# Optimization experiments

Hardware: AMD Instinct MI355X
Metric: run time of the kernel (lower is better)

The kernel has to match this reference:

```python
import jax, jax.numpy as jnp
import numpy as np

S, B, D = 2048, 2, 2048
H, C = 16, 128  # heads, dim_head
EPS = 1e-6


def _rmsnorm(x, w):
    # per-head RMSNorm, computed in float32 like the torch module
    xf = x.astype(jnp.float32)
    var = jnp.mean(xf * xf, axis=-1, keepdims=True)
    return (xf * jax.lax.rsqrt(var + EPS) * w).astype(x.dtype)


def _rope(x, freqs):
    # x: [S,B,H,C], freqs: [S,C] raw frequencies
    cos = jnp.cos(freqs)[:, None, None, :].astype(x.dtype)
    sin = jnp.sin(freqs)[:, None, None, :].astype(x.dtype)
    x1, x2 = jnp.split(x, 2, axis=-1)
    rot = jnp.concatenate((-x2, x1), axis=-1)
    return x * cos + rot * sin


def setup_inputs() -> dict:
    key = jax.random.key(0)
    ks = jax.random.split(key, 6)
    scale = 0.02
    return {
        "x": jax.random.normal(ks[0], (S, B, D), jnp.float32),
        "rope_emb": jax.random.normal(ks[1], (S, 1, 1, C), jnp.float32),
        "Wq": jax.random.normal(ks[2], (D, D), jnp.float32) * scale,
        "Wk": jax.random.normal(ks[3], (D, D), jnp.float32) * scale,
        "Wv": jax.random.normal(ks[4], (D, D), jnp.float32) * scale,
        "Wout": jax.random.normal(ks[5], (D, D), jnp.float32) * scale,
        "q_scale": jnp.ones((C,), jnp.float32),
        "k_scale": jnp.ones((C,), jnp.float32),
    }


def reference(x, rope_emb, Wq, Wk, Wv, Wout, q_scale, k_scale):
    s, b, _ = x.shape
    freqs = rope_emb.reshape(s, C)  # squeeze(1).squeeze(1)

    # QKV projections (no bias), split heads: [S,B,H,C]
    q = (x @ Wq.T).reshape(s, b, H, C)
    k = (x @ Wk.T).reshape(s, b, H, C)
    v = (x @ Wv.T).reshape(s, b, H, C)

    # per-head RMSNorm on q, k; identity on v (qkv_norm='RRI')
    q = _rmsnorm(q, q_scale)
    k = _rmsnorm(k, k_scale)

    # RoPE on q, k (self-attention)
    q = _rope(q, freqs)
    k = _rope(k, freqs)

    # SDPA, non-causal
    inv_scale = 1.0 / jnp.sqrt(jnp.asarray(C, x.dtype))
    scores = jnp.einsum('sbnc,tbnc->bnst', q, k) * inv_scale  # [B,H,S,S]
    probs = jax.nn.softmax(scores, axis=-1)
    out = jnp.einsum('bnst,tbnc->sbnc', probs, v)  # [S,B,H,C]

    # output projection (no bias, dropout inactive)
    return out.reshape(s, b, H * C) @ Wout.T
```

## Files before the change

kernel.cpp:

```cpp
#include <hip/hip_runtime.h>
#include <stdint.h>

#define S_DIM 2048
#define B_DIM 2
#define D_DIM 2048
#define H_DIM 16
#define C_DIM 128
#define M_DIM 4096

typedef __bf16 bf16x8 __attribute__((ext_vector_type(8)));
typedef float f32x4 __attribute__((ext_vector_type(4)));
typedef unsigned short u16x8 __attribute__((ext_vector_type(8)));

__device__ __forceinline__ float bf2f(unsigned short u) {
    union { unsigned int i; float f; } c; c.i = ((unsigned int)u) << 16; return c.f;
}
__device__ __forceinline__ unsigned short f2bf(float f) {
    union { float f; unsigned int i; } c; c.f = f;
    unsigned int r = c.i + 0x7FFFu + ((c.i >> 16) & 1u);
    return (unsigned short)(r >> 16);
}

__global__ void rope_tables_k(const float* __restrict__ freqs,
                              float* __restrict__ ctab, float* __restrict__ stab, int n) {
    int i = blockIdx.x * blockDim.x + threadIdx.x;
    if (i < n) { float f = freqs[i]; ctab[i] = cosf(f); stab[i] = sinf(f); }
}

__global__ void cast_all_k(const float* __restrict__ x,
                           const float* __restrict__ w0, const float* __restrict__ w1,
                           const float* __restrict__ w2, const float* __restrict__ w3,
                           unsigned short* __restrict__ xb, unsigned short* __restrict__ wb) {
    const int nx4 = (M_DIM * D_DIM) / 4;
    const int nw4 = (D_DIM * D_DIM) / 4;
    const int total = nx4 + 4 * nw4;
    int stride = gridDim.x * blockDim.x;
    for (int i = blockIdx.x * blockDim.x + threadIdx.x; i < total; i += stride) {
        const float* src; unsigned short* dst; int idx;
        if (i < nx4) { src = x; dst = xb; idx = i; }
        else {
            int j = i - nx4;
            int sel = j >> 20;
            idx = j & (nw4 - 1);
            src = (sel == 0) ? w0 : (sel == 1) ? w1 : (sel == 2) ? w2 : w3;
            dst = wb + (size_t)sel * (size_t)D_DIM * D_DIM;
        }
        float4 v = reinterpret_cast<const float4*>(src)[idx];
        ushort4 o;
        o.x = f2bf(v.x); o.y = f2bf(v.y); o.z = f2bf(v.z); o.w = f2bf(v.w);
        reinterpret_cast<ushort4*>(dst)[idx] = o;
    }
}

template <typename OutT>
__global__ __launch_bounds__(512, 2) void gemm8_k(
    const unsigned short* __restrict__ A,
    const unsigned short* __restrict__ Bm,
    OutT* __restrict__ C,
    int M, int N, int K)
{
    constexpr int TILE = 256 * 64;
    __shared__ __align__(16) unsigned short ldsA[2][TILE];
    __shared__ __align__(16) unsigned short ldsB[2][TILE];

    const int tid  = threadIdx.x;
    const int wave = tid >> 6;
    const int lane = tid & 63;
    const int wm = wave >> 2;
    const int wn = wave & 3;
    const int g  = lane >> 4;
    const int ro = lane & 15;

    const int nwg = gridDim.x * gridDim.y;
    int lin = blockIdx.y * gridDim.x + blockIdx.x;
    lin = (lin & 7) * (nwg >> 3) + (lin >> 3);
    const int brow = (lin % gridDim.x) * 256;
    const int bcol = (lin / gridDim.x) * 256;
    const int NT = K >> 6;

    const unsigned short* As = A  + (size_t)brow * K;
    const unsigned short* Bs = Bm + (size_t)bcol * K;

    f32x4 acc[8][4] = {};

    auto stageA = [&](int T) {
        const int buf = T & 1;
        #pragma unroll
        for (int j = 0; j < 4; ++j) {
            const int slot = j * 512 + tid;
            const int row = slot >> 3, c = slot & 7;
            __builtin_amdgcn_global_load_lds(
                (const __attribute__((address_space(1))) void*)(
                    As + (size_t)row * K + T * 64 + ((c ^ (row & 7)) << 3)),
                (__attribute__((address_space(3))) void*)(
                    &ldsA[buf][(j * 512 + wave * 64) * 8]),
                16, 0, 0);
        }
    };
    auto stageB = [&](int T) {
        const int buf = T & 1;
        #pragma unroll
        for (int j = 0; j < 4; ++j) {
            const int slot = j * 512 + tid;
            const int row = slot >> 3, c = slot & 7;
            __builtin_amdgcn_global_load_lds(
                (const __attribute__((address_space(1))) void*)(
                    Bs + (size_t)row * K + T * 64 + ((c ^ (row & 7)) << 3)),
                (__attribute__((address_space(3))) void*)(
                    &ldsB[buf][(j * 512 + wave * 64) * 8]),
                16, 0, 0);
        }
    };

    auto rdA = [&](int buf, int mi, int ks) -> bf16x8 {
        const int row = wm * 128 + mi * 16 + ro;
        return *reinterpret_cast<const bf16x8*>(
            &ldsA[buf][row * 64 + (((ks * 4 + g) ^ (row & 7)) << 3)]);
    };
    auto rdB = [&](int buf, int ni, int ks) -> bf16x8 {
        const int row = wn * 64 + ni * 16 + ro;
        return *reinterpret_cast<const bf16x8*>(
            &ldsB[buf][row * 64 + (((ks * 4 + g) ^ (row & 7)) << 3)]);
    };

    stageB(0);
    stageA(0);
    stageB(1);
    asm volatile("s_waitcnt vmcnt(4)" ::: "memory");
    __builtin_amdgcn_s_barrier();

    for (int T = 0; T < NT; ++T) {
        const int buf = T & 1;
        bf16x8 af[4], bfr[4];

        #pragma unroll
        for (int i = 0; i < 4; ++i) af[i] = rdA(buf, i, 0);
        #pragma unroll
        for (int i = 0; i < 4; ++i) bfr[i] = rdB(buf, i, 0);
        if (T + 1 < NT) stageA(T + 1);
        __builtin_amdgcn_s_barrier();
        asm volatile("s_waitcnt lgkmcnt(0)" ::: "memory");
        __builtin_amdgcn_sched_barrier(0);
        __builtin_amdgcn_s_setprio(1);
        #pragma unroll
        for (int mi = 0; mi < 4; ++mi)
            #pragma unroll
            for (int ni = 0; ni < 4; ++ni)
                acc[mi][ni] = __builtin_amdgcn_mfma_f32_16x16x32_bf16(af[mi], bfr[ni], acc[mi][ni], 0, 0, 0);
        __builtin_amdgcn_s_setprio(0);
        __builtin_amdgcn_s_barrier();

        #pragma unroll
        for (int i = 0; i < 4; ++i) af[i] = rdA(buf, 4 + i, 0);
        __builtin_amdgcn_s_barrier();
        asm volatile("s_waitcnt lgkmcnt(0)" ::: "memory");
        __builtin_amdgcn_sched_barrier(0);
        __builtin_amdgcn_s_setprio(1);
        #pragma unroll
        for (int mi = 0; mi < 4; ++mi)
            #pragma unroll
            for (int ni = 0; ni < 4; ++ni)
                acc[4 + mi][ni] = __builtin_amdgcn_mfma_f32_16x16x32_bf16(af[mi], bfr[ni], acc[4 + mi][ni], 0, 0, 0);
        __builtin_amdgcn_s_setprio(0);
        __builtin_amdgcn_s_barrier();

        #pragma unroll
        for (int i = 0; i < 4; ++i) af[i] = rdA(buf, i, 1);
        #pragma unroll
        for (int i = 0; i < 4; ++i) bfr[i] = rdB(buf, i, 1);
        __builtin_amdgcn_s_barrier();
        asm volatile("s_waitcnt lgkmcnt(0)" ::: "memory");
        __builtin_amdgcn_sched_barrier(0);
        __builtin_amdgcn_s_setprio(1);
        #pragma unroll
        for (int mi = 0; mi < 4; ++mi)
            #pragma unroll
            for (int ni = 0; ni < 4; ++ni)
                acc[mi][ni] = __builtin_amdgcn_mfma_f32_16x16x32_bf16(af[mi], bfr[ni], acc[mi][ni], 0, 0, 0);
        __builtin_amdgcn_s_setprio(0);
        __builtin_amdgcn_s_barrier();

        #pragma unroll
        for (int i = 0; i < 4; ++i) af[i] = rdA(buf, 4 + i, 1);
        if (T + 2 < NT) stageB(T + 2);
        if (T + 1 < NT) {
            if (T + 2 < NT) asm volatile("s_waitcnt vmcnt(4)" ::: "memory");
            else            asm volatile("s_waitcnt vmcnt(0)" ::: "memory");
        }
        __builtin_amdgcn_s_barrier();
        asm volatile("s_waitcnt lgkmcnt(0)" ::: "memory");
        __builtin_amdgcn_sched_barrier(0);
        __builtin_amdgcn_s_setprio(1);
        #pragma unroll
        for (int mi = 0; mi < 4; ++mi)
            #pragma unroll
            for (int ni = 0; ni < 4; ++ni)
                acc[4 + mi][ni] = __builtin_amdgcn_mfma_f32_16x16x32_bf16(af[mi], bfr[ni], acc[4 + mi][ni], 0, 0, 0);
        __builtin_amdgcn_s_setprio(0);
        __builtin_amdgcn_s_barrier();
    }

    const int rg = g * 4;
    #pragma unroll
    for (int mi = 0; mi < 8; ++mi) {
        #pragma unroll
        for (int r = 0; r < 4; ++r) {
            const int row = brow + wm * 128 + mi * 16 + rg + r;
            const size_t base = (size_t)row * N + bcol + wn * 64;
            #pragma unroll
            for (int ni = 0; ni < 4; ++ni) {
                float v = acc[mi][ni][r];
                if constexpr (sizeof(OutT) == 2) C[base + ni * 16 + ro] = f2bf(v);
                else                             C[base + ni * 16 + ro] = v;
            }
        }
    }
}

template <typename OutT>
__global__ __launch_bounds__(512) void gemm_v4_k(
    const unsigned short* __restrict__ A,
    const unsigned short* __restrict__ Bm,
    OutT* __restrict__ C,
    int M, int N, int K)
{
    constexpr int ATILE = 128 * 64;
    constexpr int BTILE = 256 * 64;
    __shared__ __align__(16) unsigned short ldsA[3 * ATILE];
    __shared__ __align__(16) unsigned short ldsB[3 * BTILE];

    const int tid  = threadIdx.x;
    const int wave = tid >> 6;
    const int lane = tid & 63;
    const int wm = wave >> 2;
    const int wn = wave & 3;
    const int g  = lane >> 4;
    const int ro = lane & 15;

    const int nwg = gridDim.x * gridDim.y;
    int lin = blockIdx.y * gridDim.x + blockIdx.x;
    lin = (lin & 7) * (nwg >> 3) + (lin >> 3);
    const int brow = (lin % gridDim.x) * 128;
    const int bcol = (lin / gridDim.x) * 256;
    const int NT = K >> 6;

    const unsigned short* As = A  + (size_t)brow * K;
    const unsigned short* Bs = Bm + (size_t)bcol * K;

    f32x4 acc[4][4] = {};

    auto stage = [&](int buf, int t) {
        #pragma unroll
        for (int j = 0; j < 2; ++j) {
            const int slot = j * 512 + tid;
            const int row = slot >> 3, c = slot & 7;
            __builtin_amdgcn_global_load_lds(
                (const __attribute__((address_space(1))) void*)(
                    As + (size_t)row * K + t * 64 + ((c ^ (row & 7)) << 3)),
                (__attribute__((address_space(3))) void*)(
                    ldsA + buf * ATILE + (j * 512 + wave * 64) * 8),
                16, 0, 0);
        }
        #pragma unroll
        for (int j = 0; j < 4; ++j) {
            const int slot = j * 512 + tid;
            const int row = slot >> 3, c = slot & 7;
            __builtin_amdgcn_global_load_lds(
                (const __attribute__((address_space(1))) void*)(
                    Bs + (size_t)row * K + t * 64 + ((c ^ (row & 7)) << 3)),
                (__attribute__((address_space(3))) void*)(
                    ldsB + buf * BTILE + (j * 512 + wave * 64) * 8),
                16, 0, 0);
        }
    };

    auto rdA = [&](int buf, int mi, int ks) -> bf16x8 {
        const int row = wm * 64 + mi * 16 + ro;
        const int c = (ks * 4 + g) ^ (row & 7);
        return *reinterpret_cast<const bf16x8*>(ldsA + buf * ATILE + row * 64 + c * 8);
    };
    auto rdB = [&](int buf, int ni, int ks) -> bf16x8 {
        const int row = wn * 64 + ni * 16 + ro;
        const int c = (ks * 4 + g) ^ (row & 7);
        return *reinterpret_cast<const bf16x8*>(ldsB + buf * BTILE + row * 64 + c * 8);
    };

    stage(0, 0);
    stage(1, 1);
    asm volatile("s_waitcnt vmcnt(6)" ::: "memory");
    __builtin_amdgcn_s_barrier();

    int cb = 0;
    for (int t = 0; t < NT; ++t) {
        #pragma unroll
        for (int ks = 0; ks < 2; ++ks) {
            bf16x8 af[4], bf[4];
            #pragma unroll
            for (int i = 0; i < 4; ++i) af[i] = rdA(cb, i, ks);
            #pragma unroll
            for (int i = 0; i < 4; ++i) bf[i] = rdB(cb, i, ks);
            if (ks == 0) {
                if (t + 2 < NT) stage((cb == 0) ? 2 : cb - 1, t + 2);
            } else {
                if (t + 2 < NT) asm volatile("s_waitcnt vmcnt(6)" ::: "memory");
                else            asm volatile("s_waitcnt vmcnt(0)" ::: "memory");
            }
            __builtin_amdgcn_s_barrier();
            asm volatile("s_waitcnt lgkmcnt(0)" ::: "memory");
            __builtin_amdgcn_sched_barrier(0);
            __builtin_amdgcn_s_setprio(1);
            #pragma unroll
            for (int mi = 0; mi < 4; ++mi)
                #pragma unroll
                for (int ni = 0; ni < 4; ++ni)
                    acc[mi][ni] = __builtin_amdgcn_mfma_f32_16x16x32_bf16(
                        af[mi], bf[ni], acc[mi][ni], 0, 0, 0);
            __builtin_amdgcn_s_setprio(0);
            __builtin_amdgcn_s_barrier();
        }
        cb = (cb == 2) ? 0 : cb + 1;
    }

    const int rg = g * 4;
    #pragma unroll
    for (int mi = 0; mi < 4; ++mi) {
        #pragma unroll
        for (int r = 0; r < 4; ++r) {
            const int row = brow + wm * 64 + mi * 16 + rg + r;
            const size_t base = (size_t)row * N + bcol + wn * 64;
            #pragma unroll
            for (int ni = 0; ni < 4; ++ni) {
                float v = acc[mi][ni][r];
                if constexpr (sizeof(OutT) == 2) C[base + ni * 16 + ro] = f2bf(v);
                else                             C[base + ni * 16 + ro] = v;
            }
        }
    }
}

__global__ __launch_bounds__(256) void qk_post2_k(
    const unsigned short* __restrict__ rawQKV, int ld,
    const float* __restrict__ q_scale, const float* __restrict__ k_scale,
    const float* __restrict__ ctab, const float* __restrict__ stab,
    unsigned short* __restrict__ Qb, unsigned short* __restrict__ Kb,
    float inv_scale)
{
    const int isK = blockIdx.y;
    const unsigned short* raw = rawQKV + (isK ? D_DIM : 0);
    const float* wscale = isK ? k_scale : q_scale;
    unsigned short* outp = isK ? Kb : Qb;
    const float post_mul = isK ? 1.0f : inv_scale;

    const int gw = blockIdx.x * 4 + (threadIdx.x >> 6);
    const int lane = threadIdx.x & 63;
    const int m = gw >> 4;
    const int h = gw & 15;
    const int s = m >> 1, b = m & 1;
    const int c0 = lane * 2;

    const unsigned short* src = raw + (size_t)m * ld + h * C_DIM + c0;
    unsigned int packed = *reinterpret_cast<const unsigned int*>(src);
    float x0 = bf2f((unsigned short)(packed & 0xFFFF));
    float x1 = bf2f((unsigned short)(packed >> 16));

    float ss = x0 * x0 + x1 * x1;
    #pragma unroll
    for (int off = 32; off; off >>= 1) ss += __shfl_xor(ss, off);
    const float rs = rsqrtf(ss * (1.0f / C_DIM) + 1e-6f);

    float n0 = x0 * rs * wscale[c0];
    float n1 = x1 * rs * wscale[c0 + 1];
    float p0 = __shfl_xor(n0, 32);
    float p1 = __shfl_xor(n1, 32);
    const float sgn = (lane < 32) ? -1.0f : 1.0f;
    const float* cp = ctab + (size_t)s * C_DIM + c0;
    const float* sp = stab + (size_t)s * C_DIM + c0;
    float o0 = (n0 * cp[0] + sgn * p0 * sp[0]) * post_mul;
    float o1 = (n1 * cp[1] + sgn * p1 * sp[1]) * post_mul;

    unsigned int opk = (unsigned int)f2bf(o0) | ((unsigned int)f2bf(o1) << 16);
    *reinterpret_cast<unsigned int*>(
        outp + ((size_t)(b * H_DIM + h) * S_DIM + s) * C_DIM + c0) = opk;
}

__global__ __launch_bounds__(256) void v_transpose_k(
    const unsigned short* __restrict__ raw, int ld, int colbase,
    unsigned short* __restrict__ Vt)
{
    __shared__ __align__(16) unsigned short tile[64][136];
    const int bh = blockIdx.y;
    const int b = bh >> 4, h = bh & 15;
    const int sbase = blockIdx.x * 64;
    const int t = threadIdx.x;

    {
        const int s = t >> 2, cq = (t & 3) * 32;
        const unsigned short* src = raw + (size_t)((sbase + s) * B_DIM + b) * ld + colbase + h * C_DIM + cq;
        #pragma unroll
        for (int j = 0; j < 4; ++j) {
            u16x8 v = *reinterpret_cast<const u16x8*>(src + j * 8);
            *reinterpret_cast<u16x8*>(&tile[s][cq + j * 8]) = v;
        }
    }
    __syncthreads();
    {
        const int c = t >> 1, sh = (t & 1) * 32;
        unsigned short* dst = Vt + ((size_t)bh * C_DIM + c) * S_DIM + sbase + sh;
        #pragma unroll
        for (int j = 0; j < 32; j += 8) {
            u16x8 o;
            #pragma unroll
            for (int e = 0; e < 8; ++e) o[e] = tile[sh + j + e][c];
            *reinterpret_cast<u16x8*>(dst + j) = o;
        }
    }
}

__global__ __launch_bounds__(512, 2) void attn_k(
    const unsigned short* __restrict__ Qb,
    const unsigned short* __restrict__ Kb,
    const unsigned short* __restrict__ Vt,
    unsigned short* __restrict__ Ao)
{
    __shared__ __align__(16) unsigned short ldsK[2][64 * 128];
    __shared__ __align__(16) unsigned short ldsV[2][128 * 64];
    __shared__ __align__(16) unsigned short plds[8][32 * 64];

    const int bh = blockIdx.y;
    const int wave = threadIdx.x >> 6;
    const int lane = threadIdx.x & 63;
    const int qbase = blockIdx.x * 256 + wave * 32;
    const int g  = lane >> 4;
    const int ro = lane & 15;
    const int ko = g * 8;
    const int rg = g * 4;

    const unsigned short* Q  = Qb + (size_t)bh * S_DIM * C_DIM;
    const unsigned short* Km = Kb + (size_t)bh * S_DIM * C_DIM;
    const unsigned short* V  = Vt + (size_t)bh * C_DIM * S_DIM;
    unsigned short* pw = &plds[wave][0];

    bf16x8 qf[2][4];
    #pragma unroll
    for (int mq = 0; mq < 2; ++mq)
        #pragma unroll
        for (int kf = 0; kf < 4; ++kf)
            qf[mq][kf] = *reinterpret_cast<const bf16x8*>(
                Q + (size_t)(qbase + mq * 16 + ro) * C_DIM + kf * 32 + ko);

    bf16x8 ones;
    #pragma unroll
    for (int e = 0; e < 8; ++e) ones[e] = (__bf16)1.0f;

    auto stage = [&](int bufi, int kb) {
        #pragma unroll
        for (int j = 0; j < 2; ++j) {
            const int idx = (wave * 2 + j) * 64 + lane;
            {
                const int row = idx >> 4, ch = idx & 15;
                const int sch = (ch & 8) | ((ch ^ row) & 7);
                __builtin_amdgcn_global_load_lds(
                    (const __attribute__((address_space(1))) void*)(
                        Km + (size_t)(kb + row) * C_DIM + sch * 8),
                    (__attribute__((address_space(3))) void*)(
                        &ldsK[bufi][(wave * 2 + j) * 512]),
                    16, 0, 0);
            }
            {
                const int row = idx >> 3, ch = idx & 7;
                const int sch = (ch ^ row) & 7;
                __builtin_amdgcn_global_load_lds(
                    (const __attribute__((address_space(1))) void*)(
                        V + (size_t)row * S_DIM + kb + sch * 8),
                    (__attribute__((address_space(3))) void*)(
                        &ldsV[bufi][(wave * 2 + j) * 512]),
                    16, 0, 0);
            }
        }
    };

    f32x4 of[2][8] = {};
    f32x4 osum[2] = {};
    float mrow[2][4] = {{-1e30f, -1e30f, -1e30f, -1e30f}, {-1e30f, -1e30f, -1e30f, -1e30f}};

    stage(0, 0);
    asm volatile("s_waitcnt vmcnt(0)" ::: "memory");
    __syncthreads();

    int cur = 0;
    for (int kb = 0; kb < S_DIM; kb += 64) {
        if (kb + 64 < S_DIM) stage(cur ^ 1, kb + 64);

        f32x4 s4[2][4] = {};
        __builtin_amdgcn_s_setprio(1);
        #pragma unroll
        for (int nc = 0; nc < 4; ++nc) {
            const int r_loc = nc * 16 + ro;
            bf16x8 kfr[4];
            #pragma unroll
            for (int kf = 0; kf < 4; ++kf) {
                const int c = kf * 4 + g;
                const int sch = (c & 8) | ((c ^ r_loc) & 7);
                kfr[kf] = *reinterpret_cast<const bf16x8*>(&ldsK[cur][r_loc * 128 + sch * 8]);
            }
            #pragma unroll
            for (int mq = 0; mq < 2; ++mq)
                #pragma unroll
                for (int kf = 0; kf < 4; ++kf)
                    s4[mq][nc] = __builtin_amdgcn_mfma_f32_16x16x32_bf16(
                        qf[mq][kf], kfr[kf], s4[mq][nc], 0, 0, 0);
        }
        __builtin_amdgcn_s_setprio(0);

        float mx[2][4];
        #pragma unroll
        for (int mq = 0; mq < 2; ++mq) {
            #pragma unroll
            for (int r = 0; r < 4; ++r)
                mx[mq][r] = fmaxf(fmaxf(s4[mq][0][r], s4[mq][1][r]),
                                  fmaxf(s4[mq][2][r], s4[mq][3][r]));
            #pragma unroll
            for (int off = 1; off < 16; off <<= 1)
                #pragma unroll
                for (int r = 0; r < 4; ++r) mx[mq][r] = fmaxf(mx[mq][r], __shfl_xor(mx[mq][r], off));
        }

        float mg = 0.f;
        #pragma unroll
        for (int mq = 0; mq < 2; ++mq)
            #pragma unroll
            for (int r = 0; r < 4; ++r) mg = fmaxf(mg, mx[mq][r] - mrow[mq][r]);
        if (__any(mg > 8.0f)) {
            #pragma unroll
            for (int mq = 0; mq < 2; ++mq) {
                float resc[4];
                #pragma unroll
                for (int r = 0; r < 4; ++r) {
                    float mnew = fmaxf(mrow[mq][r], mx[mq][r]);
                    resc[r] = __expf(mrow[mq][r] - mnew);
                    mrow[mq][r] = mnew;
                    osum[mq][r] *= resc[r];
                }
                #pragma unroll
                for (int nf = 0; nf < 8; ++nf)
                    #pragma unroll
                    for (int r = 0; r < 4; ++r) of[mq][nf][r] *= resc[r];
            }
        }

        #pragma unroll
        for (int mq = 0; mq < 2; ++mq)
            #pragma unroll
            for (int nc = 0; nc < 4; ++nc)
                #pragma unroll
                for (int r = 0; r < 4; ++r) {
                    float p = __expf(s4[mq][nc][r] - mrow[mq][r]);
                    const int q = mq * 16 + rg + r;
                    const int k = nc * 16 + ro;
                    pw[q * 64 + (((k >> 3) ^ (q & 7)) << 3) + (k & 7)] = f2bf(p);
                }
        __asm__ volatile("" ::: "memory");

        __builtin_amdgcn_s_setprio(1);
        #pragma unroll
        for (int ks = 0; ks < 2; ++ks) {
            bf16x8 pa[2];
            #pragma unroll
            for (int mq = 0; mq < 2; ++mq) {
                const int prow = mq * 16 + ro;
                const int psch = (ks * 4 + g) ^ (ro & 7);
                pa[mq] = *reinterpret_cast<const bf16x8*>(&pw[prow * 64 + psch * 8]);
            }
            #pragma unroll
            for (int nf = 0; nf < 8; ++nf) {
                const int vr = nf * 16 + ro;
                const int sch = (ks * 4 + g) ^ (vr & 7);
                bf16x8 vf = *reinterpret_cast<const bf16x8*>(&ldsV[cur][vr * 64 + sch * 8]);
                #pragma unroll
                for (int mq = 0; mq < 2; ++mq)
                    of[mq][nf] = __builtin_amdgcn_mfma_f32_16x16x32_bf16(pa[mq], vf, of[mq][nf], 0, 0, 0);
            }
            #pragma unroll
            for (int mq = 0; mq < 2; ++mq)
                osum[mq] = __builtin_amdgcn_mfma_f32_16x16x32_bf16(pa[mq], ones, osum[mq], 0, 0, 0);
        }
        __builtin_amdgcn_s_setprio(0);

        asm volatile("s_waitcnt vmcnt(0)" ::: "memory");
        __syncthreads();
        cur ^= 1;
    }

    const int b = bh >> 4, h = bh & 15;
    #pragma unroll
    for (int mq = 0; mq < 2; ++mq) {
        #pragma unroll
        for (int r = 0; r < 4; ++r) {
            const float inv_l = 1.0f / osum[mq][r];
            const int srow = qbase + mq * 16 + rg + r;
            unsigned short* dst = Ao + (size_t)(srow * B_DIM + b) * D_DIM + h * C_DIM;
            #pragma unroll
            for (int nf = 0; nf < 8; ++nf)
                dst[nf * 16 + ro] = f2bf(of[mq][nf][r] * inv_l);
        }
    }
}

extern "C" void kernel_launch(void* const* d_in, const int* in_sizes, int n_in,
                              void* d_out, int out_size, void* d_ws, size_t ws_size,
                              hipStream_t stream) {
    const float* x       = (const float*)d_in[0];
    const float* rope    = (const float*)d_in[1];
    const float* Wq      = (const float*)d_in[2];
    const float* Wk      = (const float*)d_in[3];
    const float* Wv      = (const float*)d_in[4];
    const float* Wo      = (const float*)d_in[5];
    const float* q_scale = (const float*)d_in[6];
    const float* k_scale = (const float*)d_in[7];
    float* out = (float*)d_out;

    char* w = (char*)d_ws;
    size_t off = 0;
    auto alloc = [&](size_t bytes) {
        char* p = w + off; off += (bytes + 255) & ~(size_t)255; return p;
    };
    unsigned short* xb   = (unsigned short*)alloc((size_t)M_DIM * D_DIM * 2);
    unsigned short* Wqb  = (unsigned short*)alloc((size_t)4 * D_DIM * D_DIM * 2);
    unsigned short* Wob  = Wqb + (size_t)3 * D_DIM * D_DIM;
    unsigned short* rawQKV = (unsigned short*)alloc((size_t)M_DIM * 3 * D_DIM * 2);
    unsigned short* Qb   = (unsigned short*)alloc((size_t)M_DIM * D_DIM * 2);
    unsigned short* Kb   = (unsigned short*)alloc((size_t)M_DIM * D_DIM * 2);
    unsigned short* Vt   = (unsigned short*)alloc((size_t)M_DIM * D_DIM * 2);
    float* ctab = (float*)alloc((size_t)S_DIM * C_DIM * 4);
    float* stab = (float*)alloc((size_t)S_DIM * C_DIM * 4);
    unsigned short* Ao = rawQKV;
    (void)ws_size; (void)in_sizes; (void)n_in; (void)out_size;

    const int NQKV = 3 * D_DIM;
    const float inv_scale = 0.08838834764831845f;

    rope_tables_k<<<(S_DIM * C_DIM + 255) / 256, 256, 0, stream>>>(rope, ctab, stab, S_DIM * C_DIM);
    cast_all_k<<<2048, 256, 0, stream>>>(x, Wq, Wk, Wv, Wo, xb, Wqb);

    gemm8_k<unsigned short><<<dim3(M_DIM / 256, NQKV / 256), 512, 0, stream>>>(
        xb, Wqb, rawQKV, M_DIM, NQKV, D_DIM);

    qk_post2_k<<<dim3(M_DIM * H_DIM / 4, 2), 256, 0, stream>>>(
        rawQKV, NQKV, q_scale, k_scale, ctab, stab, Qb, Kb, inv_scale);
    v_transpose_k<<<dim3(S_DIM / 64, B_DIM * H_DIM), 256, 0, stream>>>(rawQKV, NQKV, 2 * D_DIM, Vt);

    attn_k<<<dim3(S_DIM / 256, B_DIM * H_DIM), 512, 0, stream>>>(Qb, Kb, Vt, Ao);

    gemm_v4_k<float><<<dim3(M_DIM / 128, D_DIM / 256), 512, 0, stream>>>(
        Ao, Wob, out, M_DIM, D_DIM, D_DIM);
}
```

Measured before the change: 343.0 us.

## Widen QKV GEMM tile to 256x384 and interleave LDS reads with MFMA

```diff
diff --git a/kernel.cpp b/kernel.cpp
--- a/kernel.cpp
+++ b/kernel.cpp
@@ -52,16 +52,18 @@
     }
 }
 
-template <typename OutT>
-__global__ __launch_bounds__(512, 2) void gemm8_k(
+template <typename OutT, int BN>
+__global__ __launch_bounds__(512) void gemm8_k(
     const unsigned short* __restrict__ A,
     const unsigned short* __restrict__ Bm,
     OutT* __restrict__ C,
     int M, int N, int K)
 {
-    constexpr int TILE = 256 * 64;
-    __shared__ __align__(16) unsigned short ldsA[2][TILE];
-    __shared__ __align__(16) unsigned short ldsB[2][TILE];
+    constexpr int NFR = BN / 64;
+    constexpr int WNS = BN / 4;
+    constexpr int BCH = BN / 64 * 512;
+    __shared__ __align__(16) unsigned short ldsA[2][256 * 64];
+    __shared__ __align__(16) unsigned short ldsB[2][BN * 64];
 
     const int tid  = threadIdx.x;
     const int wave = tid >> 6;
@@ -75,13 +77,13 @@
     int lin = blockIdx.y * gridDim.x + blockIdx.x;
     lin = (lin & 7) * (nwg >> 3) + (lin >> 3);
     const int brow = (lin % gridDim.x) * 256;
-    const int bcol = (lin / gridDim.x) * 256;
+    const int bcol = (lin / gridDim.x) * BN;
     const int NT = K >> 6;
 
     const unsigned short* As = A  + (size_t)brow * K;
     const unsigned short* Bs = Bm + (size_t)bcol * K;
 
-    f32x4 acc[8][4] = {};
+    f32x4 acc[8][NFR] = {};
 
     auto stageA = [&](int T) {
         const int buf = T & 1;
@@ -100,7 +102,7 @@
     auto stageB = [&](int T) {
         const int buf = T & 1;
         #pragma unroll
-        for (int j = 0; j < 4; ++j) {
+        for (int j = 0; j < BCH / 512; ++j) {
             const int slot = j * 512 + tid;
             const int row = slot >> 3, c = slot & 7;
             __builtin_amdgcn_global_load_lds(
@@ -118,7 +120,7 @@
             &ldsA[buf][row * 64 + (((ks * 4 + g) ^ (row & 7)) << 3)]);
     };
     auto rdB = [&](int buf, int ni, int ks) -> bf16x8 {
-        const int row = wn * 64 + ni * 16 + ro;
+        const int row = wn * WNS + ni * 16 + ro;
         return *reinterpret_cast<const bf16x8*>(
             &ldsB[buf][row * 64 + (((ks * 4 + g) ^ (row & 7)) << 3)]);
     };
@@ -126,76 +128,66 @@
     stageB(0);
     stageA(0);
     stageB(1);
-    asm volatile("s_waitcnt vmcnt(4)" ::: "memory");
+    asm volatile("s_waitcnt vmcnt(6)" ::: "memory");
     __builtin_amdgcn_s_barrier();
 
     for (int T = 0; T < NT; ++T) {
         const int buf = T & 1;
-        bf16x8 af[4], bfr[4];
-
-        #pragma unroll
-        for (int i = 0; i < 4; ++i) af[i] = rdA(buf, i, 0);
-        #pragma unroll
-        for (int i = 0; i < 4; ++i) bfr[i] = rdB(buf, i, 0);
+        bf16x8 bfr[NFR];
+
+        #pragma unroll
+        for (int i = 0; i < NFR; ++i) bfr[i] = rdB(buf, i, 0);
         if (T + 1 < NT) stageA(T + 1);
         __builtin_amdgcn_s_barrier();
-        asm volatile("s_waitcnt lgkmcnt(0)" ::: "memory");
-        __builtin_amdgcn_sched_barrier(0);
         __builtin_amdgcn_s_setprio(1);
         #pragma unroll
-        for (int mi = 0; mi < 4; ++mi)
-            #pragma unroll
-            for (int ni = 0; ni < 4; ++ni)
-                acc[mi][ni] = __builtin_amdgcn_mfma_f32_16x16x32_bf16(af[mi], bfr[ni], acc[mi][ni], 0, 0, 0);
+        for (int mi = 0; mi < 4; ++mi) {
+            bf16x8 af = rdA(buf, mi, 0);
+            #pragma unroll
+            for (int ni = 0; ni < NFR; ++ni)
+                acc[mi][ni] = __builtin_amdgcn_mfma_f32_16x16x32_bf16(af, bfr[ni], acc[mi][ni], 0, 0, 0);
+        }
         __builtin_amdgcn_s_setprio(0);
         __builtin_amdgcn_s_barrier();
 
-        #pragma unroll
-        for (int i = 0; i < 4; ++i) af[i] = rdA(buf, 4 + i, 0);
-        __builtin_amdgcn_s_barrier();
-        asm volatile("s_waitcnt lgkmcnt(0)" ::: "memory");
-        __builtin_amdgcn_sched_barrier(0);
         __builtin_amdgcn_s_setprio(1);
         #pragma unroll
-        for (int mi = 0; mi < 4; ++mi)
-            #pragma unroll
-            for (int ni = 0; ni < 4; ++ni)
-                acc[4 + mi][ni] = __builtin_amdgcn_mfma_f32_16x16x32_bf16(af[mi], bfr[ni], acc[4 + mi][ni], 0, 0, 0);
+        for (int mi = 0; mi < 4; ++mi) {
+            bf16x8 af = rdA(buf, 4 + mi, 0);
+            #pragma unroll
+            for (int ni = 0; ni < NFR; ++ni)
+                acc[4 + mi][ni] = __builtin_amdgcn_mfma_f32_16x16x32_bf16(af, bfr[ni], acc[4 + mi][ni], 0, 0, 0);
+        }
         __builtin_amdgcn_s_setprio(0);
         __builtin_amdgcn_s_barrier();
 
         #pragma unroll
-        for (int i = 0; i < 4; ++i) af[i] = rdA(buf, i, 1);
-        #pragma unroll
-        for (int i = 0; i < 4; ++i) bfr[i] = rdB(buf, i, 1);
+        for (int i = 0; i < NFR; ++i) bfr[i] = rdB(buf, i, 1);
         __builtin_amdgcn_s_barrier();
-        asm volatile("s_waitcnt lgkmcnt(0)" ::: "memory");
-        __builtin_amdgcn_sched_barrier(0);
         __builtin_amdgcn_s_setprio(1);
         #pragma unroll
-        for (int mi = 0; mi < 4; ++mi)
-            #pragma unroll
-            for (int ni = 0; ni < 4; ++ni)
-                acc[mi][ni] = __builtin_amdgcn_mfma_f32_16x16x32_bf16(af[mi], bfr[ni], acc[mi][ni], 0, 0, 0);
+        for (int mi = 0; mi < 4; ++mi) {
+            bf16x8 af = rdA(buf, mi, 1);
+            #pragma unroll
+            for (int ni = 0; ni < NFR; ++ni)
+                acc[mi][ni] = __builtin_amdgcn_mfma_f32_16x16x32_bf16(af, bfr[ni], acc[mi][ni], 0, 0, 0);
+        }
         __builtin_amdgcn_s_setprio(0);
         __builtin_amdgcn_s_barrier();
 
-        #pragma unroll
-        for (int i = 0; i < 4; ++i) af[i] = rdA(buf, 4 + i, 1);
         if (T + 2 < NT) stageB(T + 2);
         if (T + 1 < NT) {
-            if (T + 2 < NT) asm volatile("s_waitcnt vmcnt(4)" ::: "memory");
+            if (T + 2 < NT) asm volatile("s_waitcnt vmcnt(6)" ::: "memory");
             else            asm volatile("s_waitcnt vmcnt(0)" ::: "memory");
         }
-        __builtin_amdgcn_s_barrier();
-        asm volatile("s_waitcnt lgkmcnt(0)" ::: "memory");
-        __builtin_amdgcn_sched_barrier(0);
         __builtin_amdgcn_s_setprio(1);
         #pragma unroll
-        for (int mi = 0; mi < 4; ++mi)
-            #pragma unroll
-            for (int ni = 0; ni < 4; ++ni)
-                acc[4 + mi][ni] = __builtin_amdgcn_mfma_f32_16x16x32_bf16(af[mi], bfr[ni], acc[4 + mi][ni], 0, 0, 0);
+        for (int mi = 0; mi < 4; ++mi) {
+            bf16x8 af = rdA(buf, 4 + mi, 1);
+            #pragma unroll
+            for (int ni = 0; ni < NFR; ++ni)
+                acc[4 + mi][ni] = __builtin_amdgcn_mfma_f32_16x16x32_bf16(af, bfr[ni], acc[4 + mi][ni], 0, 0, 0);
+        }
         __builtin_amdgcn_s_setprio(0);
         __builtin_amdgcn_s_barrier();
     }
@@ -206,9 +198,9 @@
         #pragma unroll
         for (int r = 0; r < 4; ++r) {
             const int row = brow + wm * 128 + mi * 16 + rg + r;
-            const size_t base = (size_t)row * N + bcol + wn * 64;
-            #pragma unroll
-            for (int ni = 0; ni < 4; ++ni) {
+            const size_t base = (size_t)row * N + bcol + wn * WNS;
+            #pragma unroll
+            for (int ni = 0; ni < NFR; ++ni) {
                 float v = acc[mi][ni][r];
                 if constexpr (sizeof(OutT) == 2) C[base + ni * 16 + ro] = f2bf(v);
                 else                             C[base + ni * 16 + ro] = v;
@@ -642,7 +634,7 @@
     rope_tables_k<<<(S_DIM * C_DIM + 255) / 256, 256, 0, stream>>>(rope, ctab, stab, S_DIM * C_DIM);
     cast_all_k<<<2048, 256, 0, stream>>>(x, Wq, Wk, Wv, Wo, xb, Wqb);
 
-    gemm8_k<unsigned short><<<dim3(M_DIM / 256, NQKV / 256), 512, 0, stream>>>(
+    gemm8_k<unsigned short, 384><<<dim3(M_DIM / 256, NQKV / 384), 512, 0, stream>>>(
         xb, Wqb, rawQKV, M_DIM, NQKV, D_DIM);
 
     qk_post2_k<<<dim3(M_DIM * H_DIM / 4, 2), 256, 0, stream>>>(
```

Measured after the change: 315.3 us. 8.1% less time.
